# Kernel optimization log

Measured on AMD Instinct MI355X. Metric: run time of the kernel, lower is better.

The kernel has to match this reference:

```python
import jax, jax.numpy as jnp
import numpy as np

B, L, C = 32, 128, 21
PATCH, STRIDE = 16, 16
E, H, HEADS = 128, 128, 8
NLAYERS = 2
KSIZE = 3
PRED = 96
N = (L - PATCH) // STRIDE + 1  # 8 patches


def setup_inputs() -> dict:
    key = jax.random.key(0)
    ks = jax.random.split(key, 24)
    g = lambda i, shape, s=0.05: jax.random.normal(ks[i], shape, jnp.float32) * s
    return {
        'x': g(0, (B, L, C), 1.0),
        'embed_W': g(1, (E, PATCH)), 'embed_b': g(2, (E,)),
        'ln_g': jnp.ones((E,), jnp.float32), 'ln_b': jnp.zeros((E,), jnp.float32),
        'qW': g(3, (E, E)), 'qb': g(4, (E,)),
        'kW': g(5, (E, E)), 'kb': g(6, (E,)),
        'vW': g(7, (E, E)), 'vb': g(8, (E,)),
        'lstm_Wx': g(9, (NLAYERS, 4 * H, E)), 'lstm_Wh': g(10, (NLAYERS, 4 * H, H)), 'lstm_b': g(11, (NLAYERS, 4 * H)),
        'conv_W': g(12, (E, E, KSIZE)), 'conv_b': g(13, (E,)),
        'ssm_W': g(14, (E, E)), 'ssm_b': g(15, (E,)),
        'outp_W': g(16, (E, E)), 'outp_b': g(17, (E,)),
        'proj_W': g(18, (PRED, E)), 'proj_b': g(19, (PRED,)),
    }


def _layernorm(x, g, b, eps=1e-5):
    m = x.mean(-1, keepdims=True)
    v = ((x - m) ** 2).mean(-1, keepdims=True)
    return (x - m) * jax.lax.rsqrt(v + eps) * g + b


def _xlstm_dqn(ctx, Wx, Wh, bias):
    # DQNxLSTM: re-runs a 2-layer LSTM over the FULL sequence L times,
    # carrying (h,c) across iterations; returns the outputs of the last pass.
    ctx_T = jnp.swapaxes(ctx, 0, 1)  # [N, Bc, E]
    Bc = ctx.shape[0]
    h0 = jnp.zeros((NLAYERS, Bc, H), ctx.dtype)
    c0 = jnp.zeros_like(h0)

    def cell(carry, x_t):  # x_t: [Bc, E]
        h, c = carry
        inp = x_t
        hs, cs = [], []
        for l in range(NLAYERS):
            gates = inp @ Wx[l].T + h[l] @ Wh[l].T + bias[l]  # [Bc, 4H]
            i, f, g_, o = jnp.split(gates, 4, axis=-1)
            c_new = jax.nn.sigmoid(f) * c[l] + jax.nn.sigmoid(i) * jnp.tanh(g_)
            h_new = jax.nn.sigmoid(o) * jnp.tanh(c_new)
            hs.append(h_new); cs.append(c_new)
            inp = h_new
        return (jnp.stack(hs), jnp.stack(cs)), inp

    def outer(carry, _):
        carry2, outs = jax.lax.scan(cell, carry, ctx_T)  # outs: [N, Bc, H]
        return carry2, outs

    _, all_outs = jax.lax.scan(outer, (h0, c0), None, length=N)
    return jnp.swapaxes(all_outs[-1], 0, 1)  # [Bc, N, H]


def _conv1d_same(x, W, b):  # x: [Bc, N, E]
    y = jax.lax.conv_general_dilated(
        jnp.swapaxes(x, 1, 2), W, (1,), 'SAME',
        dimension_numbers=('NCH', 'OIH', 'NCH'))
    return jnp.swapaxes(y + b[None, :, None], 1, 2)


def reference(x, embed_W, embed_b, ln_g, ln_b, qW, qb, kW, kb, vW, vb,
              lstm_Wx, lstm_Wh, lstm_b, conv_W, conv_b, ssm_W, ssm_b,
              outp_W, outp_b, proj_W, proj_b):
    Bc = B * C
    # channel independence: b l c -> (b c) l
    xc = jnp.swapaxes(x, 1, 2).reshape(Bc, L)
    # patching (unfold)
    idx = jnp.arange(N)[:, None] * STRIDE + jnp.arange(PATCH)[None, :]
    patches = xc[:, idx]  # [Bc, N, PATCH]
    emb = patches @ embed_W.T + embed_b  # [Bc, N, E]
    xn = _layernorm(emb, ln_g, ln_b)
    # attention (faithful to original, incl. scale by sqrt(E) and bhnl,bhnd->bhnd einsum)
    d = E // HEADS
    q = (xn @ qW.T + qb).reshape(Bc, N, HEADS, d).transpose(0, 2, 1, 3)
    k = (xn @ kW.T + kb).reshape(Bc, N, HEADS, d).transpose(0, 2, 1, 3)
    v = (xn @ vW.T + vb).reshape(Bc, N, HEADS, d).transpose(0, 2, 1, 3)
    attn = jax.nn.softmax(jnp.einsum('bhnd,bhld->bhnl', q, k) / (E ** 0.5), axis=-1)
    ctx = jnp.einsum('bhnl,bhnd->bhnd', attn, v)  # as in original (elementwise-in-n)
    ctx = ctx.transpose(0, 2, 1, 3).reshape(Bc, N, E)
    ctx = _xlstm_dqn(ctx, lstm_Wx, lstm_Wh, lstm_b)
    ctx = _conv1d_same(ctx, conv_W, conv_b)
    ctx = ctx @ ssm_W.T + ssm_b
    ctx = ctx @ outp_W.T + outp_b
    ctx = ctx + xn  # residual onto the normed input (as in original)
    y = ctx @ proj_W.T + proj_b  # [Bc, N, PRED]
    return y
```

## Files before the change

kernel.cpp:

```cpp
#include <hip/hip_runtime.h>

typedef unsigned short ushort_t;
typedef unsigned int uint_t;

using bf16x8 = __attribute__((ext_vector_type(8))) short;
using f32x4  = __attribute__((ext_vector_type(4))) float;

__device__ __forceinline__ ushort_t f2b(float f){
    union { float f; uint_t u; } v; v.f = f;
    uint_t u = v.u;
    uint_t r = (u + 0x7FFFu + ((u >> 16) & 1u)) >> 16;
    return (ushort_t)r;
}

__global__ void prep_k(const float* __restrict__ vW, const float* __restrict__ Wx,
                       const float* __restrict__ Wh, const float* __restrict__ cW,
                       const float* __restrict__ sW, const float* __restrict__ oW,
                       const float* __restrict__ pW, ushort_t* __restrict__ wb)
{
    int idx = blockIdx.x * 256 + threadIdx.x;
    switch (blockIdx.y){
    case 0: if (idx < 16384) wb[idx]          = f2b(vW[idx]);           break;
    case 1: if (idx < 65536) wb[16384  + idx] = f2b(Wx[idx]);           break;
    case 2: if (idx < 65536) wb[81920  + idx] = f2b(Wh[idx]);           break;
    case 3: if (idx < 65536) wb[147456 + idx] = f2b(Wx[65536 + idx]);   break;
    case 4: if (idx < 65536) wb[212992 + idx] = f2b(Wh[65536 + idx]);   break;
    case 5: if (idx < 49152){
                int k = idx >> 14; int oi = idx & 16383;
                wb[278528 + idx] = f2b(cW[oi * 3 + k]);
            } break;
    case 6: if (idx < 16384) wb[327680 + idx] = f2b(sW[idx]);           break;
    case 7: if (idx < 16384) wb[344064 + idx] = f2b(oW[idx]);           break;
    case 8: if (idx < 12288) wb[360448 + idx] = f2b(pW[idx]);           break;
    }
}

__global__ __launch_bounds__(64) void head_k(
    const float* __restrict__ x, const float* __restrict__ eW,
    const float* __restrict__ eb, const float* __restrict__ lng,
    const float* __restrict__ lnb, const ushort_t* __restrict__ vWb,
    const float* __restrict__ vb, const ushort_t* __restrict__ wx0b,
    const float* __restrict__ lb, float* __restrict__ xnF, float* __restrict__ X0F)
{
    __shared__ ushort_t xnL[2048];
    __shared__ ushort_t c0L[2048];

    const int lane = threadIdx.x;
    const int rowbase = blockIdx.x * 16;
    const int e0 = lane, e1 = lane + 64;

    float w0[16], w1[16];
#pragma unroll
    for (int p = 0; p < 16; ++p){ w0[p] = eW[e0 * 16 + p]; w1[p] = eW[e1 * 16 + p]; }
    const float bi0 = eb[e0], bi1 = eb[e1];
    const float ga0 = lng[e0], ga1 = lng[e1];
    const float be0 = lnb[e0], be1 = lnb[e1];

    for (int i = 0; i < 16; ++i){
        const int row = rowbase + i;
        const int bc = row >> 3, n = row & 7;
        const int b = bc / 21, c = bc % 21;
        const float* xp = x + (b * 128 + n * 16) * 21 + c;
        float v0 = bi0, v1 = bi1;
#pragma unroll
        for (int p = 0; p < 16; ++p){
            float pv = xp[p * 21];
            v0 += w0[p] * pv; v1 += w1[p] * pv;
        }
        float s = v0 + v1, sq = v0 * v0 + v1 * v1;
#pragma unroll
        for (int m = 32; m >= 1; m >>= 1){
            s  += __shfl_xor(s,  m);
            sq += __shfl_xor(sq, m);
        }
        float mean = s * (1.f / 128.f);
        float var  = sq * (1.f / 128.f) - mean * mean;
        float r    = rsqrtf(var + 1e-5f);
        float y0 = (v0 - mean) * r * ga0 + be0;
        float y1 = (v1 - mean) * r * ga1 + be1;
        xnF[row * 128 + e0] = y0;
        xnF[row * 128 + e1] = y1;
        const int sz = (i & 7) << 3;
        xnL[i * 128 + (e0 ^ sz)] = f2b(y0);
        xnL[i * 128 + (e1 ^ sz)] = f2b(y1);
    }

    const int r0 = lane & 15, g = lane >> 4, sw = r0 & 7;
    {
        bf16x8 a[4];
#pragma unroll
        for (int kt = 0; kt < 4; ++kt)
            a[kt] = *(const bf16x8*)(&xnL[r0 * 128 + ((kt * 32 + g * 8) ^ (sw << 3))]);
#pragma unroll
        for (int nt = 0; nt < 8; ++nt){
            const int col = nt * 16 + r0;
            float bv = vb[col];
            f32x4 acc = {bv, bv, bv, bv};
#pragma unroll
            for (int kt = 0; kt < 4; ++kt)
                acc = __builtin_amdgcn_mfma_f32_16x16x32_bf16(
                        a[kt], *(const bf16x8*)(vWb + col * 128 + kt * 32 + g * 8), acc, 0, 0, 0);
#pragma unroll
            for (int q = 0; q < 4; ++q){
                int rr = g * 4 + q;
                c0L[rr * 128 + (col ^ ((rr & 7) << 3))] = f2b(acc[q]);
            }
        }
    }
    {
        bf16x8 a[4];
#pragma unroll
        for (int kt = 0; kt < 4; ++kt)
            a[kt] = *(const bf16x8*)(&c0L[r0 * 128 + ((kt * 32 + g * 8) ^ (sw << 3))]);
        for (int nt = 0; nt < 32; ++nt){
            const int col = nt * 16 + r0;
            float bv = lb[col];
            f32x4 acc = {bv, bv, bv, bv};
#pragma unroll
            for (int kt = 0; kt < 4; ++kt)
                acc = __builtin_amdgcn_mfma_f32_16x16x32_bf16(
                        a[kt], *(const bf16x8*)(wx0b + col * 128 + kt * 32 + g * 8), acc, 0, 0, 0);
#pragma unroll
            for (int q = 0; q < 4; ++q)
                X0F[(rowbase + g * 4 + q) * 512 + col] = acc[q];
        }
    }
}

__global__ __launch_bounds__(512, 2) void lstm_f2(
    const float* __restrict__ X0, const ushort_t* __restrict__ Wh0,
    const ushort_t* __restrict__ Wx1, const ushort_t* __restrict__ Wh1,
    const float* __restrict__ lb, ushort_t* __restrict__ outB)
{
    extern __shared__ ushort_t smem[];
    ushort_t* hbuf = smem;
    ushort_t* wxs  = smem + 8192;

    const int tid = threadIdx.x;
    const int wid = tid >> 6, lane = tid & 63;
    const int r0 = lane & 15, g = lane >> 4;
    const int sw = r0 & 7;
    const int bcb = blockIdx.x * 16;
    const float K1 = 1.44269504f, K2 = 2.88539008f;

    for (int i = tid; i < 8192; i += 512) hbuf[i] = 0;
    for (int idx = tid; idx < 8192; idx += 512){
        int col = idx >> 4, c = idx & 15;
        *(bf16x8*)(wxs + col * 128 + ((c ^ (col & 7)) << 3)) =
            *(const bf16x8*)(Wx1 + col * 128 + c * 8);
    }

    bf16x8 wh0[4][4], wh1[4][4];
#pragma unroll
    for (int t4 = 0; t4 < 4; ++t4){
        const int cb = t4 * 128 + wid * 16;
#pragma unroll
        for (int kt = 0; kt < 4; ++kt){
            wh0[t4][kt] = *(const bf16x8*)(Wh0 + (cb + r0) * 128 + kt * 32 + g * 8);
            wh1[t4][kt] = *(const bf16x8*)(Wh1 + (cb + r0) * 128 + kt * 32 + g * 8);
        }
    }
    float b1v[4];
#pragma unroll
    for (int t4 = 0; t4 < 4; ++t4) b1v[t4] = lb[512 + t4 * 128 + wid * 16 + r0];

    const char* adr[4];
#pragma unroll
    for (int kt = 0; kt < 4; ++kt)
        adr[kt] = (const char*)hbuf + r0 * 256 + (((kt * 32 + g * 8) ^ (sw << 3)) << 1);
    char* wrq[4];
#pragma unroll
    for (int q = 0; q < 4; ++q){
        int row = g * 4 + q;
        wrq[q] = (char*)hbuf + row * 256 + (((wid * 16 + r0) ^ ((row & 7) << 3)) << 1);
    }
    const char* wxp[4][2];
    {
        const int e = (sw >> 2) * 64;
#pragma unroll
        for (int t4 = 0; t4 < 4; ++t4){
            const char* base = (const char*)wxs
                + (t4 * 128 + wid * 16 + r0) * 256 + ((g ^ (sw & 3)) * 16);
            wxp[t4][0] = base + e;
            wxp[t4][1] = base + (64 - e);
        }
    }
    const char* xp[4];
#pragma unroll
    for (int q = 0; q < 4; ++q)
        xp[q] = (const char*)(X0 + (bcb + g * 4 + q) * 4096 + wid * 16 + r0) + 2048;
    int tnn = 1;

    float c0[4] = {0,0,0,0}, c1[4] = {0,0,0,0};

    f32x4 acc[4];
#pragma unroll
    for (int t4 = 0; t4 < 4; ++t4)
#pragma unroll
        for (int q = 0; q < 4; ++q)
            acc[t4][q] = *(const float*)(xp[q] - 2048 + t4 * 512);

    __syncthreads();

#pragma unroll 1
    for (int tt = 0; tt < 32; ++tt){
#pragma unroll
        for (int pp = 0; pp < 2; ++pp){
            const int ph = tt * 2 + pp;
            const int RDO = (pp ^ 1) * 4096;
            const int WRO = pp * 4096;

            bf16x8 a0[4], ah[4];
#pragma unroll
            for (int kt = 0; kt < 4; ++kt){
                a0[kt] = *(const bf16x8*)(adr[kt] + RDO);
                ah[kt] = *(const bf16x8*)(adr[kt] + 8192 + RDO);
            }

#pragma unroll
            for (int kt = 0; kt < 4; ++kt)
#pragma unroll
                for (int t4 = 0; t4 < 4; ++t4)
                    acc[t4] = __builtin_amdgcn_mfma_f32_16x16x32_bf16(a0[kt], wh0[t4][kt], acc[t4], 0, 0, 0);

#pragma unroll
            for (int q = 0; q < 4; ++q){
                float iv = acc[0][q], fv = acc[1][q], gv = acc[2][q], ov = acc[3][q];
                float af = 1.f + __builtin_amdgcn_exp2f(-K1 * fv);
                float ai = 1.f + __builtin_amdgcn_exp2f(-K1 * iv);
                float bg = 1.f + __builtin_amdgcn_exp2f( K2 * gv);
                float cn = c0[q] * __builtin_amdgcn_rcpf(af)
                         + (bg - 2.f) * __builtin_amdgcn_rcpf(ai * bg);
                c0[q] = cn;
                float ao = 1.f + __builtin_amdgcn_exp2f(-K1 * ov);
                float bc = 1.f + __builtin_amdgcn_exp2f( K2 * cn);
                float hv = (bc - 2.f) * __builtin_amdgcn_rcpf(ao * bc);
                *(ushort_t*)(wrq[q] + WRO) = f2b(hv);
            }

            if (ph > 0){
                f32x4 accB[4];
#pragma unroll
                for (int t4 = 0; t4 < 4; ++t4){
                    f32x4 tmp = {b1v[t4], b1v[t4], b1v[t4], b1v[t4]};
                    accB[t4] = tmp;
                }
#pragma unroll
                for (int kt = 0; kt < 4; ++kt)
#pragma unroll
                    for (int t4 = 0; t4 < 4; ++t4){
                        bf16x8 wx = *(const bf16x8*)(wxp[t4][kt & 1] + ((kt >> 1) << 7));
                        accB[t4] = __builtin_amdgcn_mfma_f32_16x16x32_bf16(a0[kt], wx,          accB[t4], 0, 0, 0);
                        accB[t4] = __builtin_amdgcn_mfma_f32_16x16x32_bf16(ah[kt], wh1[t4][kt], accB[t4], 0, 0, 0);
                    }
#pragma unroll
                for (int q = 0; q < 4; ++q){
                    float iv = accB[0][q], fv = accB[1][q], gv = accB[2][q], ov = accB[3][q];
                    float af = 1.f + __builtin_amdgcn_exp2f(-K1 * fv);
                    float ai = 1.f + __builtin_amdgcn_exp2f(-K1 * iv);
                    float bg = 1.f + __builtin_amdgcn_exp2f( K2 * gv);
                    float cn = c1[q] * __builtin_amdgcn_rcpf(af)
                             + (bg - 2.f) * __builtin_amdgcn_rcpf(ai * bg);
                    c1[q] = cn;
                    float ao = 1.f + __builtin_amdgcn_exp2f(-K1 * ov);
                    float bc = 1.f + __builtin_amdgcn_exp2f( K2 * cn);
                    float hv = (bc - 2.f) * __builtin_amdgcn_rcpf(ao * bc);
                    *(ushort_t*)(wrq[q] + 8192 + WRO) = f2b(hv);
                    if (ph >= 57){
                        int row = g * 4 + q;
                        outB[((bcb + row) * 8 + ((ph - 1) & 7)) * 128 + wid * 16 + r0] = f2b(hv);
                    }
                }
            }

            if (ph < 63){
#pragma unroll
                for (int t4 = 0; t4 < 4; ++t4)
#pragma unroll
                    for (int q = 0; q < 4; ++q)
                        acc[t4][q] = *(const float*)(xp[q] + t4 * 512);
                long d = (tnn == 7) ? -14336L : 2048L;
                tnn = (tnn == 7) ? 0 : tnn + 1;
#pragma unroll
                for (int q = 0; q < 4; ++q) xp[q] += d;
            }
            __syncthreads();
        }
    }

    {
        bf16x8 a0[4], ah[4];
#pragma unroll
        for (int kt = 0; kt < 4; ++kt){
            a0[kt] = *(const bf16x8*)(adr[kt] + 4096);
            ah[kt] = *(const bf16x8*)(adr[kt] + 8192 + 4096);
        }
        f32x4 acc2[4];
#pragma unroll
        for (int t4 = 0; t4 < 4; ++t4){
            f32x4 tmp = {b1v[t4], b1v[t4], b1v[t4], b1v[t4]};
            acc2[t4] = tmp;
        }
#pragma unroll
        for (int kt = 0; kt < 4; ++kt)
#pragma unroll
            for (int t4 = 0; t4 < 4; ++t4){
                bf16x8 wx = *(const bf16x8*)(wxp[t4][kt & 1] + ((kt >> 1) << 7));
                acc2[t4] = __builtin_amdgcn_mfma_f32_16x16x32_bf16(a0[kt], wx,          acc2[t4], 0, 0, 0);
                acc2[t4] = __builtin_amdgcn_mfma_f32_16x16x32_bf16(ah[kt], wh1[t4][kt], acc2[t4], 0, 0, 0);
            }
#pragma unroll
        for (int q = 0; q < 4; ++q){
            float iv = acc2[0][q], fv = acc2[1][q], gv = acc2[2][q], ov = acc2[3][q];
            float af = 1.f + __builtin_amdgcn_exp2f(-K1 * fv);
            float ai = 1.f + __builtin_amdgcn_exp2f(-K1 * iv);
            float bg = 1.f + __builtin_amdgcn_exp2f( K2 * gv);
            float cn = c1[q] * __builtin_amdgcn_rcpf(af)
                     + (bg - 2.f) * __builtin_amdgcn_rcpf(ai * bg);
            float ao = 1.f + __builtin_amdgcn_exp2f(-K1 * ov);
            float bc = 1.f + __builtin_amdgcn_exp2f( K2 * cn);
            float hv = (bc - 2.f) * __builtin_amdgcn_rcpf(ao * bc);
            int row = g * 4 + q;
            outB[((bcb + row) * 8 + 7) * 128 + wid * 16 + r0] = f2b(hv);
        }
    }
}

__global__ __launch_bounds__(256) void tail_k(
    const ushort_t* __restrict__ ls, const ushort_t* __restrict__ cWk,
    const float* __restrict__ cbias, const ushort_t* __restrict__ sW,
    const float* __restrict__ sbias, const ushort_t* __restrict__ oW,
    const float* __restrict__ obias, const float* __restrict__ xnF,
    const ushort_t* __restrict__ pW, const float* __restrict__ pbias,
    float* __restrict__ out)
{
    __shared__ ushort_t bufA[8192];
    __shared__ ushort_t bufB[8192];
    const int lane = threadIdx.x & 63, wave = threadIdx.x >> 6;
    const int r0 = lane & 15, g = lane >> 4;
    const int rowbase = blockIdx.x * 64;
    const int lr0 = wave * 16;

    {
        const int n = r0 & 7;
        bf16x8 a[3][4];
#pragma unroll
        for (int k = 0; k < 3; ++k){
            bool valid = (n + k >= 1) && (n + k <= 8);
            const ushort_t* ap = ls + (rowbase + lr0 + r0 + k - 1) * 128 + g * 8;
#pragma unroll
            for (int kt = 0; kt < 4; ++kt){
                bf16x8 z = {0,0,0,0,0,0,0,0};
                a[k][kt] = valid ? *(const bf16x8*)(ap + kt * 32) : z;
            }
        }
#pragma unroll
        for (int nt = 0; nt < 8; ++nt){
            const int col = nt * 16 + r0;
            float bv = cbias[col];
            f32x4 acc = {bv, bv, bv, bv};
#pragma unroll
            for (int k = 0; k < 3; ++k)
#pragma unroll
                for (int kt = 0; kt < 4; ++kt)
                    acc = __builtin_amdgcn_mfma_f32_16x16x32_bf16(
                            a[k][kt], *(const bf16x8*)(cWk + k * 16384 + col * 128 + kt * 32 + g * 8),
                            acc, 0, 0, 0);
#pragma unroll
            for (int q = 0; q < 4; ++q){
                int row = lr0 + g * 4 + q;
                bufA[row * 128 + (col ^ ((row & 7) << 3))] = f2b(acc[q]);
            }
        }
    }
    __syncthreads();
    {
        bf16x8 a[4];
#pragma unroll
        for (int kt = 0; kt < 4; ++kt)
            a[kt] = *(const bf16x8*)(&bufA[(lr0 + r0) * 128 + ((kt * 32 + g * 8) ^ ((r0 & 7) << 3))]);
#pragma unroll
        for (int nt = 0; nt < 8; ++nt){
            const int col = nt * 16 + r0;
            float bv = sbias[col];
            f32x4 acc = {bv, bv, bv, bv};
#pragma unroll
            for (int kt = 0; kt < 4; ++kt)
                acc = __builtin_amdgcn_mfma_f32_16x16x32_bf16(
                        a[kt], *(const bf16x8*)(sW + col * 128 + kt * 32 + g * 8), acc, 0, 0, 0);
#pragma unroll
            for (int q = 0; q < 4; ++q){
                int row = lr0 + g * 4 + q;
                bufB[row * 128 + (col ^ ((row & 7) << 3))] = f2b(acc[q]);
            }
        }
    }
    __syncthreads();
    {
        bf16x8 a[4];
#pragma unroll
        for (int kt = 0; kt < 4; ++kt)
            a[kt] = *(const bf16x8*)(&bufB[(lr0 + r0) * 128 + ((kt * 32 + g * 8) ^ ((r0 & 7) << 3))]);
#pragma unroll
        for (int nt = 0; nt < 8; ++nt){
            const int col = nt * 16 + r0;
            float bv = obias[col];
            f32x4 acc = {bv, bv, bv, bv};
#pragma unroll
            for (int kt = 0; kt < 4; ++kt)
                acc = __builtin_amdgcn_mfma_f32_16x16x32_bf16(
                        a[kt], *(const bf16x8*)(oW + col * 128 + kt * 32 + g * 8), acc, 0, 0, 0);
#pragma unroll
            for (int q = 0; q < 4; ++q){
                int row = lr0 + g * 4 + q;
                float v = acc[q] + xnF[(rowbase + row) * 128 + col];
                bufA[row * 128 + (col ^ ((row & 7) << 3))] = f2b(v);
            }
        }
    }
    __syncthreads();
    {
        bf16x8 a[4];
#pragma unroll
        for (int kt = 0; kt < 4; ++kt)
            a[kt] = *(const bf16x8*)(&bufA[(lr0 + r0) * 128 + ((kt * 32 + g * 8) ^ ((r0 & 7) << 3))]);
#pragma unroll
        for (int nt = 0; nt < 6; ++nt){
            const int col = nt * 16 + r0;
            float bv = pbias[col];
            f32x4 acc = {bv, bv, bv, bv};
#pragma unroll
            for (int kt = 0; kt < 4; ++kt)
                acc = __builtin_amdgcn_mfma_f32_16x16x32_bf16(
                        a[kt], *(const bf16x8*)(pW + col * 128 + kt * 32 + g * 8), acc, 0, 0, 0);
#pragma unroll
            for (int q = 0; q < 4; ++q)
                out[(rowbase + lr0 + g * 4 + q) * 96 + col] = acc[q];
        }
    }
}

extern "C" void kernel_launch(void* const* d_in, const int* in_sizes, int n_in,
                              void* d_out, int out_size, void* d_ws, size_t ws_size,
                              hipStream_t stream)
{
    const float* x   = (const float*)d_in[0];
    const float* eW  = (const float*)d_in[1];
    const float* eb  = (const float*)d_in[2];
    const float* lng = (const float*)d_in[3];
    const float* lnb = (const float*)d_in[4];
    const float* vW  = (const float*)d_in[9];
    const float* vb  = (const float*)d_in[10];
    const float* Wx  = (const float*)d_in[11];
    const float* Wh  = (const float*)d_in[12];
    const float* lb  = (const float*)d_in[13];
    const float* cW  = (const float*)d_in[14];
    const float* cb_ = (const float*)d_in[15];
    const float* sW  = (const float*)d_in[16];
    const float* sb  = (const float*)d_in[17];
    const float* oW  = (const float*)d_in[18];
    const float* ob  = (const float*)d_in[19];
    const float* pW  = (const float*)d_in[20];
    const float* pb  = (const float*)d_in[21];

    char* ws = (char*)d_ws;
    float*    xnF = (float*)   (ws + 0);
    float*    X0F = (float*)   (ws + 5505024);
    ushort_t* lsB = (ushort_t*)(ws + 16515072);
    ushort_t* wb  = (ushort_t*)(ws + 17891328);

    hipFuncSetAttribute((const void*)lstm_f2,
                        hipFuncAttributeMaxDynamicSharedMemorySize, 147456);

    prep_k<<<dim3(256, 9), 256, 0, stream>>>(vW, Wx, Wh, cW, sW, oW, pW, wb);
    head_k<<<336, 64, 0, stream>>>(x, eW, eb, lng, lnb, wb + 0, vb, wb + 16384, lb,
                                   xnF, X0F);
    lstm_f2<<<42, 512, 147456, stream>>>(X0F, wb + 81920, wb + 147456, wb + 212992,
                                         lb, lsB);
    tail_k<<<84, 256, 0, stream>>>(lsB, wb + 278528, cb_, wb + 327680, sb,
                                   wb + 344064, ob, xnF, wb + 360448, pb, (float*)d_out);
}
```

Measured before the change: 208.4 us.

## Restructure head kernel per batch with staged input; split tail into single-wave blocks

The head kernel now runs one 256-thread block per batch element. It stages that element's input slice into shared memory before patch embedding and layernorm, then spreads the V and LSTM input-projection GEMM tiles across four waves. The tail kernel goes the other way: it uses 64-thread blocks of 16 rows, which gives 336 blocks instead of 84 for better CU coverage. The trade-off is that head_k drops to only 32 blocks on a large GPU, which may underfill it, in exchange for coalesced input reads.

```diff
diff --git a/kernel.cpp b/kernel.cpp
--- a/kernel.cpp
+++ b/kernel.cpp
@@ -35,20 +35,26 @@
     }
 }
 
-__global__ __launch_bounds__(64) void head_k(
+__global__ __launch_bounds__(256) void head_k(
     const float* __restrict__ x, const float* __restrict__ eW,
     const float* __restrict__ eb, const float* __restrict__ lng,
     const float* __restrict__ lnb, const ushort_t* __restrict__ vWb,
     const float* __restrict__ vb, const ushort_t* __restrict__ wx0b,
     const float* __restrict__ lb, float* __restrict__ xnF, float* __restrict__ X0F)
 {
-    __shared__ ushort_t xnL[2048];
-    __shared__ ushort_t c0L[2048];
-
-    const int lane = threadIdx.x;
-    const int rowbase = blockIdx.x * 16;
+    extern __shared__ char hsm[];
+    float*    xL  = (float*)hsm;
+    ushort_t* xnL = (ushort_t*)(hsm + 10752);
+    ushort_t* c0L = (ushort_t*)(hsm + 55808);
+
+    const int tid = threadIdx.x;
+    const int wv = tid >> 6, lane = tid & 63;
+    const int b = blockIdx.x;
+
+    for (int i = tid; i < 2688; i += 256) xL[i] = x[b * 2688 + i];
+    for (int i = tid; i < 1024; i += 256) xnL[168 * 128 + i] = 0;
+
     const int e0 = lane, e1 = lane + 64;
-
     float w0[16], w1[16];
 #pragma unroll
     for (int p = 0; p < 16; ++p){ w0[p] = eW[e0 * 16 + p]; w1[p] = eW[e1 * 16 + p]; }
@@ -56,11 +62,11 @@
     const float ga0 = lng[e0], ga1 = lng[e1];
     const float be0 = lnb[e0], be1 = lnb[e1];
 
-    for (int i = 0; i < 16; ++i){
-        const int row = rowbase + i;
-        const int bc = row >> 3, n = row & 7;
-        const int b = bc / 21, c = bc % 21;
-        const float* xp = x + (b * 128 + n * 16) * 21 + c;
+    __syncthreads();
+
+    for (int rc = wv; rc < 168; rc += 4){
+        const int c = rc >> 3, n = rc & 7;
+        const float* xp = &xL[(n * 16) * 21 + c];
         float v0 = bi0, v1 = bi1;
 #pragma unroll
         for (int p = 0; p < 16; ++p){
@@ -78,51 +84,55 @@
         float r    = rsqrtf(var + 1e-5f);
         float y0 = (v0 - mean) * r * ga0 + be0;
         float y1 = (v1 - mean) * r * ga1 + be1;
-        xnF[row * 128 + e0] = y0;
-        xnF[row * 128 + e1] = y1;
-        const int sz = (i & 7) << 3;
-        xnL[i * 128 + (e0 ^ sz)] = f2b(y0);
-        xnL[i * 128 + (e1 ^ sz)] = f2b(y1);
-    }
+        const int grow = b * 168 + rc;
+        xnF[grow * 128 + e0] = y0;
+        xnF[grow * 128 + e1] = y1;
+        const int sz = n << 3;
+        xnL[rc * 128 + (e0 ^ sz)] = f2b(y0);
+        xnL[rc * 128 + (e1 ^ sz)] = f2b(y1);
+    }
+    __syncthreads();
 
     const int r0 = lane & 15, g = lane >> 4, sw = r0 & 7;
-    {
+
+    for (int pi = wv; pi < 88; pi += 4){
+        const int rt = pi >> 3, nt = pi & 7;
         bf16x8 a[4];
 #pragma unroll
         for (int kt = 0; kt < 4; ++kt)
-            a[kt] = *(const bf16x8*)(&xnL[r0 * 128 + ((kt * 32 + g * 8) ^ (sw << 3))]);
-#pragma unroll
-        for (int nt = 0; nt < 8; ++nt){
-            const int col = nt * 16 + r0;
-            float bv = vb[col];
-            f32x4 acc = {bv, bv, bv, bv};
-#pragma unroll
-            for (int kt = 0; kt < 4; ++kt)
-                acc = __builtin_amdgcn_mfma_f32_16x16x32_bf16(
-                        a[kt], *(const bf16x8*)(vWb + col * 128 + kt * 32 + g * 8), acc, 0, 0, 0);
-#pragma unroll
-            for (int q = 0; q < 4; ++q){
-                int rr = g * 4 + q;
-                c0L[rr * 128 + (col ^ ((rr & 7) << 3))] = f2b(acc[q]);
-            }
-        }
-    }
-    {
+            a[kt] = *(const bf16x8*)(&xnL[(rt * 16 + r0) * 128 + ((kt * 32 + g * 8) ^ (sw << 3))]);
+        const int col = nt * 16 + r0;
+        float bv = vb[col];
+        f32x4 acc = {bv, bv, bv, bv};
+#pragma unroll
+        for (int kt = 0; kt < 4; ++kt)
+            acc = __builtin_amdgcn_mfma_f32_16x16x32_bf16(
+                    a[kt], *(const bf16x8*)(vWb + col * 128 + kt * 32 + g * 8), acc, 0, 0, 0);
+#pragma unroll
+        for (int q = 0; q < 4; ++q){
+            int rr = rt * 16 + g * 4 + q;
+            c0L[rr * 128 + (col ^ ((rr & 7) << 3))] = f2b(acc[q]);
+        }
+    }
+    __syncthreads();
+
+    for (int pi = wv; pi < 352; pi += 4){
+        const int rt = pi >> 5, nt = pi & 31;
         bf16x8 a[4];
 #pragma unroll
         for (int kt = 0; kt < 4; ++kt)
-            a[kt] = *(const bf16x8*)(&c0L[r0 * 128 + ((kt * 32 + g * 8) ^ (sw << 3))]);
-        for (int nt = 0; nt < 32; ++nt){
-            const int col = nt * 16 + r0;
-            float bv = lb[col];
-            f32x4 acc = {bv, bv, bv, bv};
-#pragma unroll
-            for (int kt = 0; kt < 4; ++kt)
-                acc = __builtin_amdgcn_mfma_f32_16x16x32_bf16(
-                        a[kt], *(const bf16x8*)(wx0b + col * 128 + kt * 32 + g * 8), acc, 0, 0, 0);
-#pragma unroll
-            for (int q = 0; q < 4; ++q)
-                X0F[(rowbase + g * 4 + q) * 512 + col] = acc[q];
+            a[kt] = *(const bf16x8*)(&c0L[(rt * 16 + r0) * 128 + ((kt * 32 + g * 8) ^ (sw << 3))]);
+        const int col = nt * 16 + r0;
+        float bv = lb[col];
+        f32x4 acc = {bv, bv, bv, bv};
+#pragma unroll
+        for (int kt = 0; kt < 4; ++kt)
+            acc = __builtin_amdgcn_mfma_f32_16x16x32_bf16(
+                    a[kt], *(const bf16x8*)(wx0b + col * 128 + kt * 32 + g * 8), acc, 0, 0, 0);
+#pragma unroll
+        for (int q = 0; q < 4; ++q){
+            int rr = rt * 16 + g * 4 + q;
+            if (rr < 168) X0F[(b * 168 + rr) * 512 + col] = acc[q];
         }
     }
 }
@@ -326,7 +336,7 @@
     }
 }
 
-__global__ __launch_bounds__(256) void tail_k(
+__global__ __launch_bounds__(64) void tail_k(
     const ushort_t* __restrict__ ls, const ushort_t* __restrict__ cWk,
     const float* __restrict__ cbias, const ushort_t* __restrict__ sW,
     const float* __restrict__ sbias, const ushort_t* __restrict__ oW,
@@ -334,12 +344,11 @@
     const ushort_t* __restrict__ pW, const float* __restrict__ pbias,
     float* __restrict__ out)
 {
-    __shared__ ushort_t bufA[8192];
-    __shared__ ushort_t bufB[8192];
-    const int lane = threadIdx.x & 63, wave = threadIdx.x >> 6;
+    __shared__ ushort_t bufA[2048];
+    __shared__ ushort_t bufB[2048];
+    const int lane = threadIdx.x;
     const int r0 = lane & 15, g = lane >> 4;
-    const int rowbase = blockIdx.x * 64;
-    const int lr0 = wave * 16;
+    const int rowbase = blockIdx.x * 16;
 
     {
         const int n = r0 & 7;
@@ -347,7 +356,7 @@
 #pragma unroll
         for (int k = 0; k < 3; ++k){
             bool valid = (n + k >= 1) && (n + k <= 8);
-            const ushort_t* ap = ls + (rowbase + lr0 + r0 + k - 1) * 128 + g * 8;
+            const ushort_t* ap = ls + (rowbase + r0 + k - 1) * 128 + g * 8;
 #pragma unroll
             for (int kt = 0; kt < 4; ++kt){
                 bf16x8 z = {0,0,0,0,0,0,0,0};
@@ -368,7 +377,7 @@
                             acc, 0, 0, 0);
 #pragma unroll
             for (int q = 0; q < 4; ++q){
-                int row = lr0 + g * 4 + q;
+                int row = g * 4 + q;
                 bufA[row * 128 + (col ^ ((row & 7) << 3))] = f2b(acc[q]);
             }
         }
@@ -378,7 +387,7 @@
         bf16x8 a[4];
 #pragma unroll
         for (int kt = 0; kt < 4; ++kt)
-            a[kt] = *(const bf16x8*)(&bufA[(lr0 + r0) * 128 + ((kt * 32 + g * 8) ^ ((r0 & 7) << 3))]);
+            a[kt] = *(const bf16x8*)(&bufA[r0 * 128 + ((kt * 32 + g * 8) ^ ((r0 & 7) << 3))]);
 #pragma unroll
         for (int nt = 0; nt < 8; ++nt){
             const int col = nt * 16 + r0;
@@ -390,7 +399,7 @@
                         a[kt], *(const bf16x8*)(sW + col * 128 + kt * 32 + g * 8), acc, 0, 0, 0);
 #pragma unroll
             for (int q = 0; q < 4; ++q){
-                int row = lr0 + g * 4 + q;
+                int row = g * 4 + q;
                 bufB[row * 128 + (col ^ ((row & 7) << 3))] = f2b(acc[q]);
             }
         }
@@ -400,7 +409,7 @@
         bf16x8 a[4];
 #pragma unroll
         for (int kt = 0; kt < 4; ++kt)
-            a[kt] = *(const bf16x8*)(&bufB[(lr0 + r0) * 128 + ((kt * 32 + g * 8) ^ ((r0 & 7) << 3))]);
+            a[kt] = *(const bf16x8*)(&bufB[r0 * 128 + ((kt * 32 + g * 8) ^ ((r0 & 7) << 3))]);
 #pragma unroll
         for (int nt = 0; nt < 8; ++nt){
             const int col = nt * 16 + r0;
@@ -412,7 +421,7 @@
                         a[kt], *(const bf16x8*)(oW + col * 128 + kt * 32 + g * 8), acc, 0, 0, 0);
 #pragma unroll
             for (int q = 0; q < 4; ++q){
-                int row = lr0 + g * 4 + q;
+                int row = g * 4 + q;
                 float v = acc[q] + xnF[(rowbase + row) * 128 + col];
                 bufA[row * 128 + (col ^ ((row & 7) << 3))] = f2b(v);
             }
@@ -423,7 +432,7 @@
         bf16x8 a[4];
 #pragma unroll
         for (int kt = 0; kt < 4; ++kt)
-            a[kt] = *(const bf16x8*)(&bufA[(lr0 + r0) * 128 + ((kt * 32 + g * 8) ^ ((r0 & 7) << 3))]);
+            a[kt] = *(const bf16x8*)(&bufA[r0 * 128 + ((kt * 32 + g * 8) ^ ((r0 & 7) << 3))]);
 #pragma unroll
         for (int nt = 0; nt < 6; ++nt){
             const int col = nt * 16 + r0;
@@ -435,7 +444,7 @@
                         a[kt], *(const bf16x8*)(pW + col * 128 + kt * 32 + g * 8), acc, 0, 0, 0);
 #pragma unroll
             for (int q = 0; q < 4; ++q)
-                out[(rowbase + lr0 + g * 4 + q) * 96 + col] = acc[q];
+                out[(rowbase + g * 4 + q) * 96 + col] = acc[q];
         }
     }
 }
@@ -471,12 +480,14 @@
 
     hipFuncSetAttribute((const void*)lstm_f2,
                         hipFuncAttributeMaxDynamicSharedMemorySize, 147456);
+    hipFuncSetAttribute((const void*)head_k,
+                        hipFuncAttributeMaxDynamicSharedMemorySize, 102400);
 
     prep_k<<<dim3(256, 9), 256, 0, stream>>>(vW, Wx, Wh, cW, sW, oW, pW, wb);
-    head_k<<<336, 64, 0, stream>>>(x, eW, eb, lng, lnb, wb + 0, vb, wb + 16384, lb,
-                                   xnF, X0F);
+    head_k<<<32, 256, 100864, stream>>>(x, eW, eb, lng, lnb, wb + 0, vb, wb + 16384, lb,
+                                        xnF, X0F);
     lstm_f2<<<42, 512, 147456, stream>>>(X0F, wb + 81920, wb + 147456, wb + 212992,
                                          lb, lsB);
-    tail_k<<<84, 256, 0, stream>>>(lsB, wb + 278528, cb_, wb + 327680, sb,
+    tail_k<<<336, 64, 0, stream>>>(lsB, wb + 278528, cb_, wb + 327680, sb,
                                    wb + 344064, ob, xnF, wb + 360448, pb, (float*)d_out);
 }
```

Measured after the change: 257.7 us. 1.24x slower.
